# Optimization experiments

Measured on AMD Instinct MI355X. Metric: run time of the kernel, lower is better.

The kernel has to match this reference:

```python
import jax, jax.numpy as jnp
import numpy as np


def setup_inputs() -> dict:
    key = jax.random.key(0)
    ks = jax.random.split(key, 8)
    B, C, L = 8, 512, 2048
    Cr = C // 8
    s = 1.0 / np.sqrt(C)
    return {
        "x": jax.random.normal(ks[0], (B, C, L), dtype=jnp.float32),
        "wq": jax.random.normal(ks[1], (Cr, C), dtype=jnp.float32) * s,
        "bq": jnp.zeros((Cr,), dtype=jnp.float32),
        "wk": jax.random.normal(ks[2], (Cr, C), dtype=jnp.float32) * s,
        "bk": jnp.zeros((Cr,), dtype=jnp.float32),
        "wv": jax.random.normal(ks[3], (C, C), dtype=jnp.float32) * s,
        "bv": jnp.zeros((C,), dtype=jnp.float32),
        "gamma": jnp.zeros((1,), dtype=jnp.float32),
    }


def reference(x, wq, bq, wk, bk, wv, bv, gamma):
    # 1x1 conv == pointwise linear over channels: [B,C,L] -> [B,Cout,L]
    q = jnp.einsum('oc,bcl->bol', wq, x) + bq[None, :, None]   # [B,C/8,L]
    k = jnp.einsum('oc,bcl->bol', wk, x) + bk[None, :, None]   # [B,C/8,L]
    v = jnp.einsum('oc,bcl->bol', wv, x) + bv[None, :, None]   # [B,C,L]
    # energy[b,i,j] = sum_d q[b,d,i] * k[b,d,j]  (no 1/sqrt(d) scaling, per source)
    energy = jnp.einsum('bdi,bdj->bij', q, k)                  # [B,L,L]
    attn = jax.nn.softmax(energy, axis=-1)                     # softmax over j
    # out[b,c,i] = sum_j v[b,c,j] * attn[b,i,j]
    out = jnp.einsum('bcj,bij->bci', v, attn)                  # [B,C,L]
    return gamma[0] * out + x
```

## Files before the change

kernel.cpp:

```cpp
#include <hip/hip_runtime.h>
#include <cmath>

#define LL  2048
#define CIN 512
#define CR  64
#define LOG2E 1.44269504088896340736f
#define M0   48.0f

typedef __bf16 bf16x8 __attribute__((ext_vector_type(8)));
typedef float f32x4 __attribute__((ext_vector_type(4)));
typedef unsigned int u32;
typedef unsigned short u16;
typedef unsigned long long u64;

__device__ __forceinline__ u16 f2bf(float f) {
  return __builtin_bit_cast(u16, (__bf16)f);
}
__device__ __forceinline__ bf16x8 ld8(const u16* p) {
  return *reinterpret_cast<const bf16x8*>(p);
}
__device__ __forceinline__ f32x4 mfma16(bf16x8 a, bf16x8 b, f32x4 c) {
  return __builtin_amdgcn_mfma_f32_16x16x32_bf16(a, b, c, 0, 0, 0);
}
__device__ __forceinline__ f32x4 mfma16f(f32x4 a, bf16x8 b, f32x4 c) {
  return __builtin_amdgcn_mfma_f32_16x16x32_bf16(__builtin_bit_cast(bf16x8, a), b, c, 0, 0, 0);
}
__device__ __forceinline__ float fexp2(float x) {
#if __has_builtin(__builtin_amdgcn_exp2f)
  return __builtin_amdgcn_exp2f(x);
#else
  return exp2f(x);
#endif
}
__device__ __forceinline__ void gload(f32x4& d, const u16* p) {
  asm volatile("global_load_dwordx4 %0, %1, off" : "=v"(d) : "v"(p));
}
#define SWAIT(N) do { \
  asm volatile("s_waitcnt vmcnt(" #N ")" ::: "memory"); \
  __builtin_amdgcn_sched_barrier(0); \
} while (0)
__device__ __forceinline__ void barrier_lds_only() {
  asm volatile("s_waitcnt lgkmcnt(0)" ::: "memory");
  __builtin_amdgcn_s_barrier();
  asm volatile("" ::: "memory");
}
__device__ __forceinline__ u16* pp(u16* base, int row, int col) {
  u32 off = ((u32)row << 8) + ((u32)col << 1);
  off ^= ((u32)(row & 7) << 4);
  return (u16*)((char*)base + off);
}
__device__ __forceinline__ const u16* ppc(const u16* base, int row, int col) {
  u32 off = ((u32)row << 8) + ((u32)col << 1);
  off ^= ((u32)(row & 7) << 4);
  return (const u16*)((const char*)base + off);
}


__global__ void cvt_weights(const float* __restrict__ wq, const float* __restrict__ wk,
                            const float* __restrict__ wv, u16* __restrict__ out) {
  int i = blockIdx.x * 256 + threadIdx.x;
  float val; int rel; u16* dst;
  if (i < CR * CIN)          { rel = i;                val = wq[rel] * LOG2E; dst = out; }
  else if (i < 2 * CR * CIN) { rel = i - CR * CIN;     val = wk[rel];         dst = out + CR * CIN; }
  else                       { rel = i - 2 * CR * CIN; val = wv[rel];         dst = out + 2 * CR * CIN; }
  const int o = rel >> 9, c = rel & 511;
  dst[(size_t)((o >> 4) * 16 + (c >> 5)) * 512 + ((c & 31) >> 3) * 128 + (o & 15) * 8 + (c & 7)] = f2bf(val);
}

__global__ __launch_bounds__(256) void xpose(const float* __restrict__ X, u16* __restrict__ xF) {
  __shared__ u16 tile[64 * 72];
  const int bb = blockIdx.z;
  const int c0 = blockIdx.y * 64;
  const int i0 = blockIdx.x * 64;
  const int t  = threadIdx.x;
  const float* Xb = X + (size_t)bb * CIN * LL;
  u32* tile32 = (u32*)tile;
#pragma unroll
  for (int r = 0; r < 8; r++) {
    int idx = t + r * 256;
    int cw = idx >> 6, i = idx & 63;
    float f0 = Xb[(size_t)(c0 + 2 * cw) * LL + i0 + i];
    float f1 = Xb[(size_t)(c0 + 2 * cw + 1) * LL + i0 + i];
    tile32[i * 36 + cw] = (u32)f2bf(f0) | ((u32)f2bf(f1) << 16);
  }
  __syncthreads();
  const int w = t >> 6, l = t & 63;
  u16* out = xF + (size_t)bb * LL * CIN;
  const int igrp0 = i0 >> 4, cg0 = c0 >> 5;
#pragma unroll
  for (int q = 0; q < 2; q++) {
    const int f  = w * 2 + q;
    const int fi = f >> 1, fc = f & 1;
    bf16x8 vv = ld8(&tile[(fi * 16 + (l & 15)) * 72 + fc * 32 + (l >> 4) * 8]);
    *(bf16x8*)(out + (size_t)((igrp0 + fi) * 16 + cg0 + fc) * 512 + l * 8) = vv;
  }
}

__global__ __launch_bounds__(256, 4) void proj_all(
    const u16* __restrict__ xF, const u16* __restrict__ wqF, const u16* __restrict__ wkF,
    const u16* __restrict__ wvF, const float* __restrict__ bq, const float* __restrict__ bk,
    const float* __restrict__ bv,
    u16* __restrict__ qT, u16* __restrict__ kF, u16* __restrict__ vF)
{
  const int bb = blockIdx.z;
  const int bx = blockIdx.x;
  const int t  = threadIdx.x;
  const int w  = t >> 6, l = t & 63;
  const int li = l & 15, g = l >> 4;
  const u16* xFb = xF + (size_t)bb * LL * CIN;

  if (bx < 64) {
    const int i0 = bx * 32;
    const int igrp0 = bx * 2;
    const int proj = w >> 1;
    const int oh = (w & 1) * 32;
    const int rg0 = oh >> 4;
    const u16* Wf = proj ? wkF : wqF;
    const float* Bs = proj ? bk : bq;
    const float bscale = proj ? 1.0f : LOG2E;

    f32x4 acc[2][2];
#pragma unroll
    for (int mt = 0; mt < 2; mt++)
#pragma unroll
      for (int nt = 0; nt < 2; nt++) acc[mt][nt] = f32x4{0.f, 0.f, 0.f, 0.f};

    bf16x8 aA[2], bA[2], aB[2], bB[2];
#define LDQK(af, bf2, cg)                                                  \
    do {                                                                   \
      af[0]  = ld8(xFb + (size_t)((igrp0    ) * 16 + (cg)) * 512 + l * 8); \
      af[1]  = ld8(xFb + (size_t)((igrp0 + 1) * 16 + (cg)) * 512 + l * 8); \
      bf2[0] = ld8(Wf  + (size_t)((rg0      ) * 16 + (cg)) * 512 + l * 8); \
      bf2[1] = ld8(Wf  + (size_t)((rg0   + 1) * 16 + (cg)) * 512 + l * 8); \
    } while (0)

    LDQK(aA, bA, 0);
#pragma unroll
    for (int cg = 0; cg < 16; cg += 2) {
      LDQK(aB, bB, cg + 1);
#pragma unroll
      for (int mt = 0; mt < 2; mt++)
#pragma unroll
        for (int nt = 0; nt < 2; nt++) acc[mt][nt] = mfma16(aA[mt], bA[nt], acc[mt][nt]);
      if (cg + 2 < 16) LDQK(aA, bA, cg + 2);
#pragma unroll
      for (int mt = 0; mt < 2; mt++)
#pragma unroll
        for (int nt = 0; nt < 2; nt++) acc[mt][nt] = mfma16(aB[mt], bB[nt], acc[mt][nt]);
    }
#undef LDQK

    if (proj == 0) {
      u16* Out = qT + (size_t)bb * LL * CR;
#pragma unroll
      for (int mt = 0; mt < 2; mt++)
#pragma unroll
        for (int nt = 0; nt < 2; nt++) {
          const int o = oh + nt * 16 + li;
          const float bias = Bs[o] * bscale;
#pragma unroll
          for (int r = 0; r < 4; r++) {
            const int i = i0 + mt * 16 + g * 4 + r;
            Out[(size_t)i * CR + o] = f2bf(acc[mt][nt][r] + bias);
          }
        }
    } else {
      u16* Out = kF + (size_t)bb * LL * CR;
      const int kk = oh >> 5;
#pragma unroll
      for (int mt = 0; mt < 2; mt++) {
        const int jgrp = (i0 >> 4) + mt;
#pragma unroll
        for (int nt = 0; nt < 2; nt++) {
          const int o = oh + nt * 16 + li;
          const float bias = Bs[o] * bscale;
          const int shi = (nt * 2 + (li >> 3)) * 16;
          const int e   = li & 7;
#pragma unroll
          for (int r = 0; r < 4; r++) {
            const int slot = shi + g * 4 + r;
            Out[(size_t)(jgrp * 2 + kk) * 512 + slot * 8 + e] = f2bf(acc[mt][nt][r] + bias);
          }
        }
      }
    }
  } else {
    const int vx = bx - 64;
    const int i0 = (vx & 31) * 64;
    const int o0 = (vx >> 5) * 64;
    const int igrp_v = (i0 >> 4) + w;
    const int rgv0 = o0 >> 4;

    f32x4 acc[4];
#pragma unroll
    for (int mt = 0; mt < 4; mt++) acc[mt] = f32x4{0.f, 0.f, 0.f, 0.f};

    bf16x8 xA, aA[4], xB, aB[4];
#define LDV(xf, af, cg)                                                      \
    do {                                                                     \
      xf    = ld8(xFb + (size_t)(igrp_v * 16 + (cg)) * 512 + l * 8);         \
      af[0] = ld8(wvF + (size_t)((rgv0    ) * 16 + (cg)) * 512 + l * 8);     \
      af[1] = ld8(wvF + (size_t)((rgv0 + 1) * 16 + (cg)) * 512 + l * 8);     \
      af[2] = ld8(wvF + (size_t)((rgv0 + 2) * 16 + (cg)) * 512 + l * 8);     \
      af[3] = ld8(wvF + (size_t)((rgv0 + 3) * 16 + (cg)) * 512 + l * 8);     \
    } while (0)

    LDV(xA, aA, 0);
#pragma unroll
    for (int cg = 0; cg < 16; cg += 2) {
      LDV(xB, aB, cg + 1);
#pragma unroll
      for (int mt = 0; mt < 4; mt++) acc[mt] = mfma16(aA[mt], xA, acc[mt]);
      if (cg + 2 < 16) LDV(xA, aA, cg + 2);
#pragma unroll
      for (int mt = 0; mt < 4; mt++) acc[mt] = mfma16(aB[mt], xB, acc[mt]);
    }
#undef LDV

    u16* Vb = vF + (size_t)bb * CIN * LL;
    const int jg2 = (i0 >> 5) + (w >> 1);
    const int gg  = (w & 1) * 2 + (li >> 3);
    const int e   = li & 7;
#pragma unroll
    for (int mt = 0; mt < 4; mt++) {
      const int cgrp = (o0 >> 4) + mt;
#pragma unroll
      for (int r = 0; r < 4; r++) {
        const int o = o0 + mt * 16 + g * 4 + r;
        const int slot = gg * 16 + (g * 4 + r);
        Vb[(size_t)(cgrp * 64 + jg2) * 512 + slot * 8 + e] = f2bf(acc[mt][r] + bv[o]);
      }
    }
  }
}

__global__ __launch_bounds__(512, 2) void attn_mfma(
    const u16* __restrict__ qT, const u16* __restrict__ kF, const u16* __restrict__ vF,
    const float* __restrict__ X, const float* __restrict__ Gamma, float* __restrict__ Y,
    int nb)
{
  __shared__ u16 Pls[2][64 * 128];
  __shared__ float lsb[8][64];
  const int bid  = blockIdx.x;
  const int bb   = bid % nb;
  const int i0   = (bid / nb) * 64;
  const int t    = threadIdx.x;
  const int w    = t >> 6, l = t & 63;
  const int li   = l & 15, g = l >> 4;
  const int c0   = w * 64;
  const int cg0  = c0 >> 4;
  const u16* qTb = qT + (size_t)bb * LL * CR;
  const u16* kFb = kF + (size_t)bb * LL * CR;
  const u16* vFb = vF + (size_t)bb * CIN * LL;

  bf16x8 qf[4][2];
#pragma unroll
  for (int ni = 0; ni < 4; ni++)
#pragma unroll
    for (int kk = 0; kk < 2; kk++)
      qf[ni][kk] = ld8(qTb + (size_t)(i0 + ni * 16 + li) * CR + kk * 32 + g * 8);

  f32x4 acc[4][4];
#pragma unroll
  for (int mC = 0; mC < 4; mC++)
#pragma unroll
    for (int ni = 0; ni < 4; ni++) acc[mC][ni] = f32x4{0.f, 0.f, 0.f, 0.f};
  float lsum[4] = {0.f, 0.f, 0.f, 0.f};

  f32x4 kf0, kf1;
  f32x4 vA[4], vB[4], vC[4], vD[4];
  gload(kf0, kFb + (size_t)(w * 2 + 0) * 512 + l * 8);
  gload(kf1, kFb + (size_t)(w * 2 + 1) * 512 + l * 8);
#pragma unroll
  for (int mC = 0; mC < 4; mC++)
    gload(vA[mC], vFb + (size_t)((cg0 + mC) * 64 + 0) * 512 + l * 8);
#pragma unroll
  for (int mC = 0; mC < 4; mC++)
    gload(vB[mC], vFb + (size_t)((cg0 + mC) * 64 + 1) * 512 + l * 8);

#pragma unroll 1
  for (int jt = 0; jt < LL; jt += 128) {
    u16* Pbuf = Pls[(jt >> 7) & 1];
    const int jn  = (jt + 128 < LL) ? jt + 128 : 0;
    const int jg  = jt >> 5;
    const int jgn = jn >> 5;

    SWAIT(8);
    f32x4 s[4];
#pragma unroll
    for (int ni = 0; ni < 4; ni++) {
      s[ni] = mfma16f(kf0, qf[ni][0], f32x4{0.f, 0.f, 0.f, 0.f});
      s[ni] = mfma16f(kf1, qf[ni][1], s[ni]);
    }
#pragma unroll
    for (int mC = 0; mC < 4; mC++)
      gload(vC[mC], vFb + (size_t)((cg0 + mC) * 64 + jg + 2) * 512 + l * 8);
#pragma unroll
    for (int mC = 0; mC < 4; mC++)
      gload(vD[mC], vFb + (size_t)((cg0 + mC) * 64 + jg + 3) * 512 + l * 8);
    gload(kf0, kFb + (size_t)((((jn >> 4) + w) * 2 + 0)) * 512 + l * 8);
    gload(kf1, kFb + (size_t)((((jn >> 4) + w) * 2 + 1)) * 512 + l * 8);

    const int colb = w * 16 + g * 4;
#pragma unroll
    for (int ni = 0; ni < 4; ni++) {
      const float e0 = fexp2(s[ni][0] - M0);
      const float e1 = fexp2(s[ni][1] - M0);
      const float e2 = fexp2(s[ni][2] - M0);
      const float e3 = fexp2(s[ni][3] - M0);
      lsum[ni] += (e0 + e1) + (e2 + e3);
      u32 lo = (u32)f2bf(e0) | ((u32)f2bf(e1) << 16);
      u32 hi = (u32)f2bf(e2) | ((u32)f2bf(e3) << 16);
      *(u64*)pp(Pbuf, ni * 16 + li, colb) = ((u64)hi << 32) | lo;
    }

    barrier_lds_only();

    bf16x8 pf[4];
#pragma unroll
    for (int ni = 0; ni < 4; ni++) pf[ni] = ld8(ppc(Pbuf, ni * 16 + li, 0 * 32 + g * 8));
    SWAIT(14);
    __builtin_amdgcn_s_setprio(1);
#pragma unroll
    for (int mC = 0; mC < 4; mC++)
#pragma unroll
      for (int ni = 0; ni < 4; ni++) acc[mC][ni] = mfma16f(vA[mC], pf[ni], acc[mC][ni]);
    __builtin_amdgcn_s_setprio(0);
#pragma unroll
    for (int mC = 0; mC < 4; mC++)
      gload(vA[mC], vFb + (size_t)((cg0 + mC) * 64 + jgn + 0) * 512 + l * 8);
#pragma unroll
    for (int ni = 0; ni < 4; ni++) pf[ni] = ld8(ppc(Pbuf, ni * 16 + li, 1 * 32 + g * 8));
    SWAIT(14);
    __builtin_amdgcn_s_setprio(1);
#pragma unroll
    for (int mC = 0; mC < 4; mC++)
#pragma unroll
      for (int ni = 0; ni < 4; ni++) acc[mC][ni] = mfma16f(vB[mC], pf[ni], acc[mC][ni]);
    __builtin_amdgcn_s_setprio(0);
#pragma unroll
    for (int mC = 0; mC < 4; mC++)
      gload(vB[mC], vFb + (size_t)((cg0 + mC) * 64 + jgn + 1) * 512 + l * 8);
#pragma unroll
    for (int ni = 0; ni < 4; ni++) pf[ni] = ld8(ppc(Pbuf, ni * 16 + li, 2 * 32 + g * 8));
    SWAIT(14);
    __builtin_amdgcn_s_setprio(1);
#pragma unroll
    for (int mC = 0; mC < 4; mC++)
#pragma unroll
      for (int ni = 0; ni < 4; ni++) acc[mC][ni] = mfma16f(vC[mC], pf[ni], acc[mC][ni]);
    __builtin_amdgcn_s_setprio(0);
#pragma unroll
    for (int ni = 0; ni < 4; ni++) pf[ni] = ld8(ppc(Pbuf, ni * 16 + li, 3 * 32 + g * 8));
    SWAIT(10);
    __builtin_amdgcn_s_setprio(1);
#pragma unroll
    for (int mC = 0; mC < 4; mC++)
#pragma unroll
      for (int ni = 0; ni < 4; ni++) acc[mC][ni] = mfma16f(vD[mC], pf[ni], acc[mC][ni]);
    __builtin_amdgcn_s_setprio(0);
  }
  SWAIT(0);

#pragma unroll
  for (int ni = 0; ni < 4; ni++) {
    lsum[ni] += __shfl_xor(lsum[ni], 16);
    lsum[ni] += __shfl_xor(lsum[ni], 32);
  }
  if (g == 0) {
#pragma unroll
    for (int ni = 0; ni < 4; ni++) lsb[w][ni * 16 + li] = lsum[ni];
  }
  __syncthreads();
  float linv[4];
#pragma unroll
  for (int ni = 0; ni < 4; ni++) {
    const int i = ni * 16 + li;
    float s8 = lsb[0][i] + lsb[1][i] + lsb[2][i] + lsb[3][i]
             + lsb[4][i] + lsb[5][i] + lsb[6][i] + lsb[7][i];
    linv[ni] = 1.0f / s8;
  }

  const float gamma = Gamma[0];
  const float* Xb = X + (size_t)bb * CIN * LL;
  float*       Yb = Y + (size_t)bb * CIN * LL;
#pragma unroll
  for (int mC = 0; mC < 4; mC++)
#pragma unroll
    for (int ni = 0; ni < 4; ni++)
#pragma unroll
      for (int r = 0; r < 4; r++) {
        const int c = c0 + mC * 16 + g * 4 + r;
        const int i = i0 + ni * 16 + li;
        const size_t off = (size_t)c * LL + i;
        Yb[off] = gamma * acc[mC][ni][r] * linv[ni] + Xb[off];
      }
}

extern "C" void kernel_launch(void* const* d_in, const int* in_sizes, int n_in,
                              void* d_out, int out_size, void* d_ws, size_t ws_size,
                              hipStream_t stream) {
  const float* x  = (const float*)d_in[0];
  const float* wq = (const float*)d_in[1];
  const float* bq = (const float*)d_in[2];
  const float* wk = (const float*)d_in[3];
  const float* bk = (const float*)d_in[4];
  const float* wv = (const float*)d_in[5];
  const float* bv = (const float*)d_in[6];
  const float* gm = (const float*)d_in[7];
  float* y = (float*)d_out;

  u16* wqF = (u16*)d_ws;
  u16* wkF = wqF + (size_t)CR * CIN;
  u16* wvF = wkF + (size_t)CR * CIN;
  u16* dyn = wvF + (size_t)CIN * CIN;
  const size_t wbytes = ((size_t)2 * CR * CIN + (size_t)CIN * CIN) * 2;
  const size_t perb = ((size_t)LL * CIN + 2 * (size_t)LL * CR + (size_t)CIN * LL);
  int nbc = 8;
  while (nbc > 1 && ws_size < wbytes + perb * 2 * (size_t)nbc) nbc >>= 1;

  const dim3 blk(256, 1, 1);
  const int nw = 2 * CR * CIN + CIN * CIN;
  hipLaunchKernelGGL(cvt_weights, dim3((nw + 255) / 256), blk, 0, stream, wq, wk, wv, wqF);

  for (int b0 = 0; b0 < 8; b0 += nbc) {
    const int nb = (8 - b0 < nbc) ? (8 - b0) : nbc;
    u16* xF = dyn;
    u16* qT = xF + (size_t)nb * LL * CIN;
    u16* kF = qT + (size_t)nb * LL * CR;
    u16* vF = kF + (size_t)nb * LL * CR;
    const float* xb = x + (size_t)b0 * CIN * LL;
    float*       yb = y + (size_t)b0 * CIN * LL;

    hipLaunchKernelGGL(xpose, dim3(LL / 64, CIN / 64, nb), blk, 0, stream, xb, xF);
    hipLaunchKernelGGL(proj_all, dim3(320, 1, nb), blk, 0, stream,
                       xF, wqF, wkF, wvF, bq, bk, bv, qT, kF, vF);
    hipLaunchKernelGGL(attn_mfma, dim3(32 * nb, 1, 1), dim3(512, 1, 1), 0, stream,
                       qT, kF, vF, xb, gm, yb, nb);
  }
}
```

Baseline: 94.06 us.

## Retile attention blocks to 256 query rows by 128 channels for V reuse

Each attention block now covers 256 query positions and a quarter of the output channels instead of 64 positions and all 512 channels. Each loaded V fragment therefore feeds four times as many query rows, which cuts V global traffic. The cost is that QK^T and the exp/softmax numerators are recomputed once per channel quarter. The P staging buffer grows to 128 KB of LDS, and the row-sum reduction becomes two-way instead of eight-way.

```diff
diff --git a/kernel.cpp b/kernel.cpp
--- a/kernel.cpp
+++ b/kernel.cpp
@@ -239,16 +239,21 @@
     const float* __restrict__ X, const float* __restrict__ Gamma, float* __restrict__ Y,
     int nb)
 {
-  __shared__ u16 Pls[2][64 * 128];
-  __shared__ float lsb[8][64];
+  __shared__ u16 Pls[2][256 * 128];
+  __shared__ float lsb[2][256];
   const int bid  = blockIdx.x;
   const int bb   = bid % nb;
-  const int i0   = (bid / nb) * 64;
+  const int rest = bid / nb;
+  const int i0   = (rest >> 2) * 256;
+  const int ch   = (rest & 3) * 128;
   const int t    = threadIdx.x;
   const int w    = t >> 6, l = t & 63;
   const int li   = l & 15, g = l >> 4;
-  const int c0   = w * 64;
-  const int cg0  = c0 >> 4;
+  const int jh   = w & 1;
+  const int qq   = w >> 1;
+  const int pc   = w & 3;
+  const int ph   = w >> 2;
+  const int cg0  = (ch >> 4) + pc * 2;
   const u16* qTb = qT + (size_t)bb * LL * CR;
   const u16* kFb = kF + (size_t)bb * LL * CR;
   const u16* vFb = vF + (size_t)bb * CIN * LL;
@@ -258,24 +263,25 @@
   for (int ni = 0; ni < 4; ni++)
 #pragma unroll
     for (int kk = 0; kk < 2; kk++)
-      qf[ni][kk] = ld8(qTb + (size_t)(i0 + ni * 16 + li) * CR + kk * 32 + g * 8);
-
-  f32x4 acc[4][4];
-#pragma unroll
-  for (int mC = 0; mC < 4; mC++)
-#pragma unroll
-    for (int ni = 0; ni < 4; ni++) acc[mC][ni] = f32x4{0.f, 0.f, 0.f, 0.f};
+      qf[ni][kk] = ld8(qTb + (size_t)(i0 + qq * 64 + ni * 16 + li) * CR + kk * 32 + g * 8);
+  SWAIT(0);
+
+  f32x4 acc[2][8];
+#pragma unroll
+  for (int mC = 0; mC < 2; mC++)
+#pragma unroll
+    for (int ni = 0; ni < 8; ni++) acc[mC][ni] = f32x4{0.f, 0.f, 0.f, 0.f};
   float lsum[4] = {0.f, 0.f, 0.f, 0.f};
 
-  f32x4 kf0, kf1;
-  f32x4 vA[4], vB[4], vC[4], vD[4];
-  gload(kf0, kFb + (size_t)(w * 2 + 0) * 512 + l * 8);
-  gload(kf1, kFb + (size_t)(w * 2 + 1) * 512 + l * 8);
-#pragma unroll
-  for (int mC = 0; mC < 4; mC++)
+  f32x4 kA[8], vA[2], vB[2], vC[2], vD[2];
+#pragma unroll
+  for (int mtk = 0; mtk < 8; mtk++)
+    gload(kA[mtk], kFb + (size_t)((jh * 4 + (mtk >> 1)) * 2 + (mtk & 1)) * 512 + l * 8);
+#pragma unroll
+  for (int mC = 0; mC < 2; mC++)
     gload(vA[mC], vFb + (size_t)((cg0 + mC) * 64 + 0) * 512 + l * 8);
 #pragma unroll
-  for (int mC = 0; mC < 4; mC++)
+  for (int mC = 0; mC < 2; mC++)
     gload(vB[mC], vFb + (size_t)((cg0 + mC) * 64 + 1) * 512 + l * 8);
 
 #pragma unroll 1
@@ -285,80 +291,75 @@
     const int jg  = jt >> 5;
     const int jgn = jn >> 5;
 
-    SWAIT(8);
-    f32x4 s[4];
-#pragma unroll
-    for (int ni = 0; ni < 4; ni++) {
-      s[ni] = mfma16f(kf0, qf[ni][0], f32x4{0.f, 0.f, 0.f, 0.f});
-      s[ni] = mfma16f(kf1, qf[ni][1], s[ni]);
+    SWAIT(4);
+#pragma unroll
+    for (int mt = 0; mt < 4; mt++) {
+      f32x4 s[4];
+#pragma unroll
+      for (int ni = 0; ni < 4; ni++) {
+        s[ni] = mfma16f(kA[mt * 2 + 0], qf[ni][0], f32x4{0.f, 0.f, 0.f, 0.f});
+        s[ni] = mfma16f(kA[mt * 2 + 1], qf[ni][1], s[ni]);
+      }
+      const int colb = jh * 64 + mt * 16 + g * 4;
+#pragma unroll
+      for (int ni = 0; ni < 4; ni++) {
+        const float e0 = fexp2(s[ni][0] - M0);
+        const float e1 = fexp2(s[ni][1] - M0);
+        const float e2 = fexp2(s[ni][2] - M0);
+        const float e3 = fexp2(s[ni][3] - M0);
+        lsum[ni] += (e0 + e1) + (e2 + e3);
+        u32 lo = (u32)f2bf(e0) | ((u32)f2bf(e1) << 16);
+        u32 hi = (u32)f2bf(e2) | ((u32)f2bf(e3) << 16);
+        *(u64*)pp(Pbuf, qq * 64 + ni * 16 + li, colb) = ((u64)hi << 32) | lo;
+      }
     }
 #pragma unroll
-    for (int mC = 0; mC < 4; mC++)
+    for (int mC = 0; mC < 2; mC++)
       gload(vC[mC], vFb + (size_t)((cg0 + mC) * 64 + jg + 2) * 512 + l * 8);
 #pragma unroll
-    for (int mC = 0; mC < 4; mC++)
+    for (int mC = 0; mC < 2; mC++)
       gload(vD[mC], vFb + (size_t)((cg0 + mC) * 64 + jg + 3) * 512 + l * 8);
-    gload(kf0, kFb + (size_t)((((jn >> 4) + w) * 2 + 0)) * 512 + l * 8);
-    gload(kf1, kFb + (size_t)((((jn >> 4) + w) * 2 + 1)) * 512 + l * 8);
-
-    const int colb = w * 16 + g * 4;
-#pragma unroll
-    for (int ni = 0; ni < 4; ni++) {
-      const float e0 = fexp2(s[ni][0] - M0);
-      const float e1 = fexp2(s[ni][1] - M0);
-      const float e2 = fexp2(s[ni][2] - M0);
-      const float e3 = fexp2(s[ni][3] - M0);
-      lsum[ni] += (e0 + e1) + (e2 + e3);
-      u32 lo = (u32)f2bf(e0) | ((u32)f2bf(e1) << 16);
-      u32 hi = (u32)f2bf(e2) | ((u32)f2bf(e3) << 16);
-      *(u64*)pp(Pbuf, ni * 16 + li, colb) = ((u64)hi << 32) | lo;
-    }
+#pragma unroll
+    for (int mtk = 0; mtk < 8; mtk++)
+      gload(kA[mtk], kFb + (size_t)(((jn >> 4) + jh * 4 + (mtk >> 1)) * 2 + (mtk & 1)) * 512 + l * 8);
 
     barrier_lds_only();
 
-    bf16x8 pf[4];
-#pragma unroll
-    for (int ni = 0; ni < 4; ni++) pf[ni] = ld8(ppc(Pbuf, ni * 16 + li, 0 * 32 + g * 8));
-    SWAIT(14);
-    __builtin_amdgcn_s_setprio(1);
-#pragma unroll
-    for (int mC = 0; mC < 4; mC++)
-#pragma unroll
-      for (int ni = 0; ni < 4; ni++) acc[mC][ni] = mfma16f(vA[mC], pf[ni], acc[mC][ni]);
-    __builtin_amdgcn_s_setprio(0);
-#pragma unroll
-    for (int mC = 0; mC < 4; mC++)
+#define PV_STEP(VX, KS, WAITN)                                                   \
+    do {                                                                         \
+      bf16x8 pf[4];                                                              \
+      _Pragma("unroll")                                                          \
+      for (int ni = 0; ni < 4; ni++)                                             \
+        pf[ni] = ld8(ppc(Pbuf, ph * 128 + ni * 16 + li, (KS) * 32 + g * 8));     \
+      SWAIT(WAITN);                                                              \
+      __builtin_amdgcn_s_setprio(1);                                             \
+      _Pragma("unroll")                                                          \
+      for (int mC = 0; mC < 2; mC++)                                             \
+        _Pragma("unroll")                                                        \
+        for (int ni = 0; ni < 4; ni++)                                           \
+          acc[mC][ni] = mfma16f(VX[mC], pf[ni], acc[mC][ni]);                    \
+      _Pragma("unroll")                                                          \
+      for (int ni = 0; ni < 4; ni++)                                             \
+        pf[ni] = ld8(ppc(Pbuf, ph * 128 + (ni + 4) * 16 + li, (KS) * 32 + g * 8));\
+      _Pragma("unroll")                                                          \
+      for (int mC = 0; mC < 2; mC++)                                             \
+        _Pragma("unroll")                                                        \
+        for (int ni = 0; ni < 4; ni++)                                           \
+          acc[mC][ni + 4] = mfma16f(VX[mC], pf[ni], acc[mC][ni + 4]);            \
+      __builtin_amdgcn_s_setprio(0);                                             \
+    } while (0)
+
+    PV_STEP(vA, 0, 14);
+#pragma unroll
+    for (int mC = 0; mC < 2; mC++)
       gload(vA[mC], vFb + (size_t)((cg0 + mC) * 64 + jgn + 0) * 512 + l * 8);
-#pragma unroll
-    for (int ni = 0; ni < 4; ni++) pf[ni] = ld8(ppc(Pbuf, ni * 16 + li, 1 * 32 + g * 8));
-    SWAIT(14);
-    __builtin_amdgcn_s_setprio(1);
-#pragma unroll
-    for (int mC = 0; mC < 4; mC++)
-#pragma unroll
-      for (int ni = 0; ni < 4; ni++) acc[mC][ni] = mfma16f(vB[mC], pf[ni], acc[mC][ni]);
-    __builtin_amdgcn_s_setprio(0);
-#pragma unroll
-    for (int mC = 0; mC < 4; mC++)
+    PV_STEP(vB, 1, 14);
+#pragma unroll
+    for (int mC = 0; mC < 2; mC++)
       gload(vB[mC], vFb + (size_t)((cg0 + mC) * 64 + jgn + 1) * 512 + l * 8);
-#pragma unroll
-    for (int ni = 0; ni < 4; ni++) pf[ni] = ld8(ppc(Pbuf, ni * 16 + li, 2 * 32 + g * 8));
-    SWAIT(14);
-    __builtin_amdgcn_s_setprio(1);
-#pragma unroll
-    for (int mC = 0; mC < 4; mC++)
-#pragma unroll
-      for (int ni = 0; ni < 4; ni++) acc[mC][ni] = mfma16f(vC[mC], pf[ni], acc[mC][ni]);
-    __builtin_amdgcn_s_setprio(0);
-#pragma unroll
-    for (int ni = 0; ni < 4; ni++) pf[ni] = ld8(ppc(Pbuf, ni * 16 + li, 3 * 32 + g * 8));
-    SWAIT(10);
-    __builtin_amdgcn_s_setprio(1);
-#pragma unroll
-    for (int mC = 0; mC < 4; mC++)
-#pragma unroll
-      for (int ni = 0; ni < 4; ni++) acc[mC][ni] = mfma16f(vD[mC], pf[ni], acc[mC][ni]);
-    __builtin_amdgcn_s_setprio(0);
+    PV_STEP(vC, 2, 14);
+    PV_STEP(vD, 3, 12);
+#undef PV_STEP
   }
   SWAIT(0);
 
@@ -369,32 +370,27 @@
   }
   if (g == 0) {
 #pragma unroll
-    for (int ni = 0; ni < 4; ni++) lsb[w][ni * 16 + li] = lsum[ni];
+    for (int ni = 0; ni < 4; ni++) lsb[jh][qq * 64 + ni * 16 + li] = lsum[ni];
   }
   __syncthreads();
-  float linv[4];
-#pragma unroll
-  for (int ni = 0; ni < 4; ni++) {
-    const int i = ni * 16 + li;
-    float s8 = lsb[0][i] + lsb[1][i] + lsb[2][i] + lsb[3][i]
-             + lsb[4][i] + lsb[5][i] + lsb[6][i] + lsb[7][i];
-    linv[ni] = 1.0f / s8;
-  }
 
   const float gamma = Gamma[0];
   const float* Xb = X + (size_t)bb * CIN * LL;
   float*       Yb = Y + (size_t)bb * CIN * LL;
 #pragma unroll
-  for (int mC = 0; mC < 4; mC++)
-#pragma unroll
-    for (int ni = 0; ni < 4; ni++)
+  for (int ni = 0; ni < 8; ni++) {
+    const int q = ph * 128 + ni * 16 + li;
+    const float linv = 1.0f / (lsb[0][q] + lsb[1][q]);
+    const int i = i0 + q;
+#pragma unroll
+    for (int mC = 0; mC < 2; mC++)
 #pragma unroll
       for (int r = 0; r < 4; r++) {
-        const int c = c0 + mC * 16 + g * 4 + r;
-        const int i = i0 + ni * 16 + li;
+        const int c = ch + pc * 32 + mC * 16 + g * 4 + r;
         const size_t off = (size_t)c * LL + i;
-        Yb[off] = gamma * acc[mC][ni][r] * linv[ni] + Xb[off];
+        Yb[off] = gamma * acc[mC][ni][r] * linv + Xb[off];
       }
+  }
 }
 
 extern "C" void kernel_launch(void* const* d_in, const int* in_sizes, int n_in,
```

After: 111.9 us. 1.19x slower.
